# Kernel optimization log

Measured on AMD Instinct MI355X. Metric: run time of the kernel, lower is better.

The kernel has to match this reference:

```python
import jax, jax.numpy as jnp
import numpy as np

T, B, IN_DIM = 512, 256, 256
H1, H = 512, 256          # fc hidden, GRU hidden
OUT_DIM = 18


def setup_inputs() -> dict:
    key = jax.random.key(0)
    ks = jax.random.split(key, 14)
    s = 0.05
    return {
        "x":      jax.random.normal(ks[0], (T, B, IN_DIM), dtype=jnp.float32),
        # fc1: Linear(IN_DIM,H1)+ReLU, Linear(H1,H)+ReLU
        "W_fc1a": jax.random.normal(ks[1], (H1, IN_DIM), dtype=jnp.float32) * s,
        "b_fc1a": jax.random.normal(ks[2], (H1,), dtype=jnp.float32) * s,
        "W_fc1b": jax.random.normal(ks[3], (H, H1), dtype=jnp.float32) * s,
        "b_fc1b": jax.random.normal(ks[4], (H,), dtype=jnp.float32) * s,
        # GRUCell(H, H): weights ordered [r, z, n] like torch
        "W_ih":   jax.random.normal(ks[5], (3 * H, H), dtype=jnp.float32) * s,
        "b_ih":   jax.random.normal(ks[6], (3 * H,), dtype=jnp.float32) * s,
        "W_hh":   jax.random.normal(ks[7], (3 * H, H), dtype=jnp.float32) * s,
        "b_hh":   jax.random.normal(ks[8], (3 * H,), dtype=jnp.float32) * s,
        # fc2: Linear(H,H1)+ReLU, Linear(H1,OUT_DIM)
        "W_fc2a": jax.random.normal(ks[9], (H1, H), dtype=jnp.float32) * s,
        "b_fc2a": jax.random.normal(ks[10], (H1,), dtype=jnp.float32) * s,
        "W_fc2b": jax.random.normal(ks[11], (OUT_DIM, H1), dtype=jnp.float32) * s,
        "b_fc2b": jax.random.normal(ks[12], (OUT_DIM,), dtype=jnp.float32) * s,
    }


def reference(x, W_fc1a, b_fc1a, W_fc1b, b_fc1b,
              W_ih, b_ih, W_hh, b_hh,
              W_fc2a, b_fc2a, W_fc2b, b_fc2b):
    batch = x.shape[1]
    h0 = jnp.zeros((batch, W_hh.shape[1]), dtype=x.dtype)

    def step(h, xt):
        # fc1 MLP
        a = jax.nn.relu(xt @ W_fc1a.T + b_fc1a)
        a = jax.nn.relu(a @ W_fc1b.T + b_fc1b)
        # GRUCell (torch gate order r, z, n)
        gi = a @ W_ih.T + b_ih            # [B, 3H]
        gh = h @ W_hh.T + b_hh            # [B, 3H]
        i_r, i_z, i_n = jnp.split(gi, 3, axis=-1)
        h_r, h_z, h_n = jnp.split(gh, 3, axis=-1)
        r = jax.nn.sigmoid(i_r + h_r)
        z = jax.nn.sigmoid(i_z + h_z)
        n = jnp.tanh(i_n + r * h_n)
        h_new = (1.0 - z) * n + z * h
        # fc2 head
        q = jax.nn.relu(h_new @ W_fc2a.T + b_fc2a) @ W_fc2b.T + b_fc2b
        return h_new, q

    _, qs = jax.lax.scan(step, h0, x)     # qs: [T, B, OUT_DIM]
    return qs
```

## Files before the change

### kernel.cpp

```cpp
#include <hip/hip_runtime.h>
#include <hip/hip_fp16.h>
#include <cstdio>

typedef unsigned short u16;
typedef __attribute__((ext_vector_type(8))) _Float16 f16x8;
typedef __attribute__((ext_vector_type(4))) float fv4;

#define TT 512
#define BB 256

__device__ __forceinline__ float us2f(u16 u) {
    union { u16 u; _Float16 h; } c; c.u = u; return (float)c.h;
}
__device__ __forceinline__ u16 f2us(float f) {
    union { u16 u; _Float16 h; } c; c.h = (_Float16)f; return c.u;
}

__device__ __forceinline__ void gl_lds16(const u16* g, u16* l) {
    __builtin_amdgcn_global_load_lds(
        (const __attribute__((address_space(1))) void*)g,
        (__attribute__((address_space(3))) void*)l, 16, 0, 0);
}

__global__ void cvt_f32_f16(const float* __restrict__ s, u16* __restrict__ d, int n) {
    long stride = (long)gridDim.x * blockDim.x * 8;
    for (long i = ((long)blockIdx.x * blockDim.x + threadIdx.x) * 8; i < n; i += stride) {
        f16x8 o;
#pragma unroll
        for (int j = 0; j < 8; ++j) o[j] = (_Float16)s[i + j];
        *(f16x8*)(d + i) = o;
    }
}

__global__ void bias_fold(const float* __restrict__ bih, const float* __restrict__ bhh,
                          float* __restrict__ bsum) {
    int i = blockIdx.x * blockDim.x + threadIdx.x;
    if (i < 768) bsum[i] = bih[i] + (i < 512 ? bhh[i] : 0.f);
}

__global__ void pack_whh(const float* __restrict__ W, u16* __restrict__ Wp) {
    int t = blockIdx.x * blockDim.x + threadIdx.x;
    int l = t & 63;
    int kt = (t >> 6) & 7;
    int jt = t >> 9;
    int j = jt * 16 + (l & 15);
    int k = kt * 32 + (l >> 4) * 8;
    f16x8 o;
#pragma unroll
    for (int i = 0; i < 8; ++i) o[i] = (_Float16)W[j * 256 + k + i];
    *(f16x8*)(Wp + (size_t)t * 8) = o;
}

__global__ void pack_w2b(const float* __restrict__ W, u16* __restrict__ Wp) {
    int t = blockIdx.x * blockDim.x + threadIdx.x;
    int l = t & 63;
    int kt = (t >> 6) & 15;
    int nt = t >> 10;
    int n = nt * 16 + (l & 15);
    int k = kt * 32 + (l >> 4) * 8;
    f16x8 o;
#pragma unroll
    for (int i = 0; i < 8; ++i)
        o[i] = (n < 18) ? (_Float16)W[n * 512 + k + i] : (_Float16)0.f;
    *(f16x8*)(Wp + (size_t)t * 8) = o;
}

__global__ __launch_bounds__(256) void gemm_bt(
    const u16* __restrict__ A, const u16* __restrict__ B,
    const float* __restrict__ bias, u16* __restrict__ C,
    int N, int K, int act)
{
    __shared__ u16 Ash[4096] __attribute__((aligned(16)));
    __shared__ u16 Bsh[4096] __attribute__((aligned(16)));
    const int tid = threadIdx.x;
    const int l = tid & 63, w = tid >> 6;
    const long m0 = (long)blockIdx.y * 128;
    const int n0 = blockIdx.x * 128;
    const int r = tid >> 2, c8 = (tid & 3) * 8;
    const u16* gA0 = A + (m0 + r) * K + c8;
    const u16* gA1 = A + (m0 + 64 + r) * K + c8;
    const u16* gB0 = B + (long)(n0 + r) * K + c8;
    const u16* gB1 = B + (long)(n0 + 64 + r) * K + c8;
    const int mb = (w >> 1) * 64, nb = (w & 1) * 64;
    const int mrow = l & 15, colq = (l >> 4) * 8;
    fv4 acc[4][4] = {};
    for (int k0 = 0; k0 < K; k0 += 32) {
        gl_lds16(gA0 + k0, &Ash[tid * 8]);
        gl_lds16(gA1 + k0, &Ash[2048 + tid * 8]);
        gl_lds16(gB0 + k0, &Bsh[tid * 8]);
        gl_lds16(gB1 + k0, &Bsh[2048 + tid * 8]);
        __syncthreads();
        f16x8 af[4], bf[4];
#pragma unroll
        for (int i = 0; i < 4; ++i)
            af[i] = *(const f16x8*)&Ash[(mb + i * 16 + mrow) * 32 + colq];
#pragma unroll
        for (int i = 0; i < 4; ++i)
            bf[i] = *(const f16x8*)&Bsh[(nb + i * 16 + mrow) * 32 + colq];
#pragma unroll
        for (int mt = 0; mt < 4; ++mt)
#pragma unroll
            for (int nt = 0; nt < 4; ++nt)
                acc[mt][nt] = __builtin_amdgcn_mfma_f32_16x16x32_f16(
                    af[mt], bf[nt], acc[mt][nt], 0, 0, 0);
        __syncthreads();
    }
    float bv[4];
#pragma unroll
    for (int nt = 0; nt < 4; ++nt) bv[nt] = bias[n0 + nb + nt * 16 + mrow];
    const int rq = (l >> 4) * 4;
#pragma unroll
    for (int mt = 0; mt < 4; ++mt)
#pragma unroll
        for (int nt = 0; nt < 4; ++nt)
#pragma unroll
            for (int i = 0; i < 4; ++i) {
                float v = acc[mt][nt][i] + bv[nt];
                if (act) v = fmaxf(v, 0.f);
                C[(m0 + mb + mt * 16 + rq + i) * (long)N + (n0 + nb + nt * 16 + mrow)] = f2us(v);
            }
}

__global__ __launch_bounds__(256) void gemm_gi(
    const u16* __restrict__ A, const u16* __restrict__ B,
    const float* __restrict__ bias, u16* __restrict__ GIp)
{
    __shared__ u16 Ash[4096] __attribute__((aligned(16)));
    __shared__ u16 Bsh[4096] __attribute__((aligned(16)));
    const int tid = threadIdx.x;
    const int l = tid & 63, w = tid >> 6;
    const long m0 = (long)blockIdx.y * 128;
    const int n0 = blockIdx.x * 128;
    const int r = tid >> 2, c8 = (tid & 3) * 8;
    const u16* gA0 = A + (m0 + r) * 256 + c8;
    const u16* gA1 = A + (m0 + 64 + r) * 256 + c8;
    const u16* gB0 = B + (long)(n0 + r) * 256 + c8;
    const u16* gB1 = B + (long)(n0 + 64 + r) * 256 + c8;
    const int mb = (w >> 1) * 64, nb = (w & 1) * 64;
    const int mrow = l & 15, colq = (l >> 4) * 8;
    fv4 acc[4][4] = {};
    for (int k0 = 0; k0 < 256; k0 += 32) {
        gl_lds16(gA0 + k0, &Ash[tid * 8]);
        gl_lds16(gA1 + k0, &Ash[2048 + tid * 8]);
        gl_lds16(gB0 + k0, &Bsh[tid * 8]);
        gl_lds16(gB1 + k0, &Bsh[2048 + tid * 8]);
        __syncthreads();
        f16x8 af[4], bf[4];
#pragma unroll
        for (int i = 0; i < 4; ++i)
            af[i] = *(const f16x8*)&Ash[(mb + i * 16 + mrow) * 32 + colq];
#pragma unroll
        for (int i = 0; i < 4; ++i)
            bf[i] = *(const f16x8*)&Bsh[(nb + i * 16 + mrow) * 32 + colq];
#pragma unroll
        for (int mt = 0; mt < 4; ++mt)
#pragma unroll
            for (int nt = 0; nt < 4; ++nt)
                acc[mt][nt] = __builtin_amdgcn_mfma_f32_16x16x32_f16(
                    af[mt], bf[nt], acc[mt][nt], 0, 0, 0);
        __syncthreads();
    }
    float bv[4];
#pragma unroll
    for (int nt = 0; nt < 4; ++nt) bv[nt] = bias[n0 + nb + nt * 16 + mrow];
    const int rq = (l >> 4) * 4;
#pragma unroll
    for (int mt = 0; mt < 4; ++mt)
#pragma unroll
        for (int nt = 0; nt < 4; ++nt)
#pragma unroll
            for (int i = 0; i < 4; ++i) {
                float v = acc[mt][nt][i] + bv[nt];
                int m = (int)(m0 + mb + mt * 16 + rq + i);
                int n = n0 + nb + nt * 16 + mrow;
                int t  = m >> 8, b = m & 255;
                int blk = b >> 4, rb = b & 15, q = rb >> 2, i2 = rb & 3;
                int g = n >> 8, c = n & 255, w2 = c >> 5, s = (c >> 4) & 1, cl = c & 15;
                size_t idx = ((((size_t)t * 16 + blk) * 8 + w2) * 64 + (q * 16 + cl)) * 24
                             + (g * 2 + s) * 4 + i2;
                GIp[idx] = f2us(v);
            }
}

__global__ __launch_bounds__(512, 2) void gru_seq5(
    const u16* __restrict__ Wp, const u16* __restrict__ GIp,
    const float* __restrict__ bhh, u16* __restrict__ Hp)
{
    __shared__ u16 h_sh[2][4096] __attribute__((aligned(16)));
    __shared__ u16 Wl[49152] __attribute__((aligned(16)));
    const int tid = threadIdx.x;
    const int l = tid & 63, w = tid >> 6;
    const int blk = blockIdx.x;
    const int col = l & 15, quad = l >> 4;

    for (int i = tid; i < 4096; i += 512) h_sh[0][i] = 0;
    for (int idx = tid; idx < 6144; idx += 512) {
        int kt6 = idx / 3072, rem = idx % 3072;
        *(f16x8*)&Wl[(size_t)idx * 8] =
            *(const f16x8*)&Wp[(((size_t)(rem >> 6) * 8 + 6 + kt6) * 64 + (rem & 63)) * 8];
    }

    int jts[6];
#pragma unroll
    for (int g = 0; g < 3; ++g)
#pragma unroll
        for (int s = 0; s < 2; ++s) jts[g * 2 + s] = g * 16 + 2 * w + s;

    f16x8 wf[6][6];
#pragma unroll
    for (int u = 0; u < 6; ++u)
#pragma unroll
        for (int kt = 0; kt < 6; ++kt)
            wf[u][kt] = *(const f16x8*)&Wp[(((size_t)jts[u] * 8 + kt) * 64 + l) * 8];
#pragma unroll
    for (int u = 0; u < 6; ++u)
#pragma unroll
        for (int kt = 0; kt < 6; ++kt)
            asm volatile("" : "+v"(wf[u][kt]));

    float hbn[2] = { bhh[512 + 32 * w + col], bhh[512 + 32 * w + 16 + col] };

    const u16* gbase = GIp + ((size_t)(blk * 8 + w) * 64 + l) * 24;
    f16x8 gcur[3], gnxt[3];
#pragma unroll
    for (int j = 0; j < 3; ++j) gcur[j] = *(const f16x8*)(gbase + j * 8);

    float hold[2][4] = {};
    u16* hp_base = Hp + (size_t)blk * 4096 + tid * 8;
    __syncthreads();

    for (int t = 0; t < TT; ++t) {
        const int rd = t & 1, wr = (t + 1) & 1;
        if (t) {
            f16x8 hv = *(const f16x8*)&h_sh[rd][tid * 8];
            *(f16x8*)(hp_base + (size_t)(t - 1) * 65536) = hv;
        }
        const u16* gn = gbase + (size_t)(t < TT - 1 ? t + 1 : t) * 196608;
#pragma unroll
        for (int j = 0; j < 3; ++j) gnxt[j] = *(const f16x8*)(gn + j * 8);

        fv4 acc[6] = {};
#pragma unroll
        for (int kt = 0; kt < 6; ++kt) {
            f16x8 a = *(const f16x8*)&h_sh[rd][(kt * 64 + l) * 8];
#pragma unroll
            for (int u = 0; u < 6; ++u)
                acc[u] = __builtin_amdgcn_mfma_f32_16x16x32_f16(a, wf[u][kt], acc[u], 0, 0, 0);
        }
#pragma unroll
        for (int kt6 = 0; kt6 < 2; ++kt6) {
            f16x8 a = *(const f16x8*)&h_sh[rd][((6 + kt6) * 64 + l) * 8];
#pragma unroll
            for (int u = 0; u < 6; ++u) {
                f16x8 bw = *(const f16x8*)&Wl[((size_t)(kt6 * 48 + jts[u]) * 64 + l) * 8];
                acc[u] = __builtin_amdgcn_mfma_f32_16x16x32_f16(a, bw, acc[u], 0, 0, 0);
            }
        }
#pragma unroll
        for (int s = 0; s < 2; ++s) {
            const int q2 = s * 2 + (col >> 3);
#pragma unroll
            for (int i = 0; i < 4; ++i) {
                float pr  = (float)gcur[0][s * 4 + i] + acc[0 + s][i];
                float pz  = (float)gcur[1][s * 4 + i] + acc[2 + s][i];
                float h_n = acc[4 + s][i] + hbn[s];
                float rg = __builtin_amdgcn_rcpf(1.f + __expf(-pr));
                float zg = __builtin_amdgcn_rcpf(1.f + __expf(-pz));
                float pre = (float)gcur[2][s * 4 + i] + rg * h_n;
                float ea = __expf(-2.f * fabsf(pre));
                float th = (1.f - ea) * __builtin_amdgcn_rcpf(1.f + ea);
                float ng = (pre >= 0.f) ? th : -th;
                float hn = (1.f - zg) * ng + zg * hold[s][i];
                hold[s][i] = hn;
                h_sh[wr][(w * 64 + q2 * 16 + quad * 4 + i) * 8 + (col & 7)] = f2us(hn);
            }
        }
#pragma unroll
        for (int j = 0; j < 3; ++j) gcur[j] = gnxt[j];
        __syncthreads();
    }
    {
        f16x8 hv = *(const f16x8*)&h_sh[0][tid * 8];
        *(f16x8*)(hp_base + (size_t)511 * 65536) = hv;
    }
}

__global__ __launch_bounds__(256) void gemm_hp(
    const u16* __restrict__ Hp, const u16* __restrict__ B,
    const float* __restrict__ bias, u16* __restrict__ C)
{
    __shared__ u16 Bsh[4096] __attribute__((aligned(16)));
    const int tid = threadIdx.x;
    const int l = tid & 63, w = tid >> 6;
    const long m0 = (long)blockIdx.y * 128;
    const int n0 = blockIdx.x * 128;
    const int r = tid >> 2, c8 = (tid & 3) * 8;
    const u16* gB0 = B + (long)(n0 + r) * 256 + c8;
    const u16* gB1 = B + (long)(n0 + 64 + r) * 256 + c8;
    const int mb = (w >> 1) * 64, nb = (w & 1) * 64;
    const int mrow = l & 15, colq = (l >> 4) * 8;
    const int t = (int)(m0 >> 8), half = ((int)m0 >> 7) & 1;
    const u16* aBase = Hp + ((size_t)t * 16 + half * 8 + (mb >> 4)) * 4096 + (size_t)l * 8;
    fv4 acc[4][4] = {};
    for (int k0 = 0; k0 < 256; k0 += 32) {
        gl_lds16(gB0 + k0, &Bsh[tid * 8]);
        gl_lds16(gB1 + k0, &Bsh[2048 + tid * 8]);
        const int kt = k0 >> 5;
        f16x8 af[4];
#pragma unroll
        for (int i = 0; i < 4; ++i)
            af[i] = *(const f16x8*)(aBase + (size_t)i * 4096 + kt * 512);
        __syncthreads();
        f16x8 bf[4];
#pragma unroll
        for (int i = 0; i < 4; ++i)
            bf[i] = *(const f16x8*)&Bsh[(nb + i * 16 + mrow) * 32 + colq];
#pragma unroll
        for (int mt = 0; mt < 4; ++mt)
#pragma unroll
            for (int nt = 0; nt < 4; ++nt)
                acc[mt][nt] = __builtin_amdgcn_mfma_f32_16x16x32_f16(
                    af[mt], bf[nt], acc[mt][nt], 0, 0, 0);
        __syncthreads();
    }
    float bv[4];
#pragma unroll
    for (int nt = 0; nt < 4; ++nt) bv[nt] = bias[n0 + nb + nt * 16 + mrow];
    const int rq = (l >> 4) * 4;
#pragma unroll
    for (int mt = 0; mt < 4; ++mt)
#pragma unroll
        for (int nt = 0; nt < 4; ++nt)
#pragma unroll
            for (int i = 0; i < 4; ++i) {
                float v = fmaxf(acc[mt][nt][i] + bv[nt], 0.f);
                C[(m0 + mb + mt * 16 + rq + i) * 512L + (n0 + nb + nt * 16 + mrow)] = f2us(v);
            }
}

__global__ __launch_bounds__(256) void head_gemm(
    const u16* __restrict__ Q1, const u16* __restrict__ W2p,
    const float* __restrict__ b2, float* __restrict__ out)
{
    __shared__ u16 Ash[4096] __attribute__((aligned(16)));
    __shared__ u16 Bsh[16384] __attribute__((aligned(16)));
    const int tid = threadIdx.x;
    const int l = tid & 63, w = tid >> 6;
    const long m0 = (long)blockIdx.x * 128;
    const int col = l & 15, quad = l >> 4, colq = quad * 8;
    for (int i = tid * 8; i < 16384; i += 2048)
        *(f16x8*)&Bsh[i] = *(const f16x8*)&W2p[i];
    const int r = tid >> 2, c8 = (tid & 3) * 8;
    const u16* gA0 = Q1 + (m0 + r) * 512 + c8;
    const u16* gA1 = Q1 + (m0 + 64 + r) * 512 + c8;
    fv4 acc[2][2] = {};
    for (int k0 = 0; k0 < 512; k0 += 32) {
        gl_lds16(gA0 + k0, &Ash[tid * 8]);
        gl_lds16(gA1 + k0, &Ash[2048 + tid * 8]);
        __syncthreads();
        const int kt = k0 >> 5;
        f16x8 af[2], bf[2];
#pragma unroll
        for (int mt = 0; mt < 2; ++mt)
            af[mt] = *(const f16x8*)&Ash[(w * 32 + mt * 16 + col) * 32 + colq];
#pragma unroll
        for (int nt = 0; nt < 2; ++nt)
            bf[nt] = *(const f16x8*)&Bsh[((nt * 16 + kt) * 64 + l) * 8];
#pragma unroll
        for (int mt = 0; mt < 2; ++mt)
#pragma unroll
            for (int nt = 0; nt < 2; ++nt)
                acc[mt][nt] = __builtin_amdgcn_mfma_f32_16x16x32_f16(
                    af[mt], bf[nt], acc[mt][nt], 0, 0, 0);
        __syncthreads();
    }
    const int rq = quad * 4;
#pragma unroll
    for (int nt = 0; nt < 2; ++nt) {
        int c = nt * 16 + col;
        if (c < 18) {
            float bias = b2[c];
#pragma unroll
            for (int mt = 0; mt < 2; ++mt)
#pragma unroll
                for (int i = 0; i < 4; ++i)
                    out[(m0 + w * 32 + mt * 16 + rq + i) * 18 + c] = acc[mt][nt][i] + bias;
        }
    }
}

extern "C" void kernel_launch(void* const* d_in, const int* in_sizes, int n_in,
                              void* d_out, int out_size, void* d_ws, size_t ws_size,
                              hipStream_t stream) {
    const float* x   = (const float*)d_in[0];
    const float* W1a = (const float*)d_in[1];
    const float* b1a = (const float*)d_in[2];
    const float* W1b = (const float*)d_in[3];
    const float* b1b = (const float*)d_in[4];
    const float* Wih = (const float*)d_in[5];
    const float* bih = (const float*)d_in[6];
    const float* Whh = (const float*)d_in[7];
    const float* bhh = (const float*)d_in[8];
    const float* W2a = (const float*)d_in[9];
    const float* b2a = (const float*)d_in[10];
    const float* W2b = (const float*)d_in[11];
    const float* b2b = (const float*)d_in[12];

    char* ws = (char*)d_ws;
    u16* R    = (u16*)ws;
    u16* A2b  = (u16*)(ws + 201326592);
    u16* XH   = (u16*)(ws + 268435456);
    float* bsum = (float*)(ws + 268435456 + 67108864 - 4096);
    u16* W1ah = (u16*)(ws + 335544320);
    u16* W1bh = (u16*)(ws + 335806464);
    u16* Wihh = (u16*)(ws + 336068608);
    u16* W2ah = (u16*)(ws + 336461824);
    u16* Wpk  = (u16*)(ws + 336723968);
    u16* W2p  = (u16*)(ws + 337117184);
    if (ws_size < 337149952) {
        fprintf(stderr, "kernel_launch: ws too small (%zu < 337149952)\n", ws_size);
    }

    cvt_f32_f16<<<dim3(2048), dim3(256), 0, stream>>>(x, XH, 33554432);
    cvt_f32_f16<<<dim3(64), dim3(256), 0, stream>>>(W1a, W1ah, 131072);
    cvt_f32_f16<<<dim3(64), dim3(256), 0, stream>>>(W1b, W1bh, 131072);
    cvt_f32_f16<<<dim3(96), dim3(256), 0, stream>>>(Wih, Wihh, 196608);
    cvt_f32_f16<<<dim3(64), dim3(256), 0, stream>>>(W2a, W2ah, 131072);
    pack_whh<<<dim3(96), dim3(256), 0, stream>>>(Whh, Wpk);
    pack_w2b<<<dim3(8), dim3(256), 0, stream>>>(W2b, W2p);

    gemm_bt<<<dim3(4, 1024), dim3(256), 0, stream>>>(XH, W1ah, b1a, R,   512, 256, 1);
    bias_fold<<<dim3(3), dim3(256), 0, stream>>>(bih, bhh, bsum);
    gemm_bt<<<dim3(2, 1024), dim3(256), 0, stream>>>(R,  W1bh, b1b, A2b, 256, 512, 1);
    gemm_gi<<<dim3(6, 1024), dim3(256), 0, stream>>>(A2b, Wihh, bsum, R);
    gru_seq5<<<dim3(16), dim3(512), 0, stream>>>(Wpk, R, bhh, XH);
    gemm_hp<<<dim3(4, 1024), dim3(256), 0, stream>>>(XH, W2ah, b2a, R);
    head_gemm<<<dim3(1024), dim3(256), 0, stream>>>(R, W2p, b2b, (float*)d_out);
}
```

Before: 1.569 ms.

## Split GRU recurrent step across 16 waves per block instead of 8

The sequential GRU kernel now launches 1024 threads per block, so each wave owns one 16-column tile per gate instead of two. Per-wave register weights halve, MFMA chains per step shrink from 48 to 24, and the gate loads narrow to 4-wide halves. The tanh is also rewritten in a cheaper exp/rcp form and the state update becomes a single fma-style blend. This shortens the per-timestep critical path of the latency-bound recurrence, at the cost of a barrier over twice as many waves each step.

```diff
diff --git a/kernel.cpp b/kernel.cpp
--- a/kernel.cpp
+++ b/kernel.cpp
@@ -4,6 +4,7 @@
 
 typedef unsigned short u16;
 typedef __attribute__((ext_vector_type(8))) _Float16 f16x8;
+typedef __attribute__((ext_vector_type(4))) _Float16 f16x4;
 typedef __attribute__((ext_vector_type(4))) float fv4;
 
 #define TT 512
@@ -182,7 +183,7 @@
             }
 }
 
-__global__ __launch_bounds__(512, 2) void gru_seq5(
+__global__ __launch_bounds__(1024) void gru_seq7(
     const u16* __restrict__ Wp, const u16* __restrict__ GIp,
     const float* __restrict__ bhh, u16* __restrict__ Hp)
 {
@@ -193,93 +194,85 @@
     const int blk = blockIdx.x;
     const int col = l & 15, quad = l >> 4;
 
-    for (int i = tid; i < 4096; i += 512) h_sh[0][i] = 0;
-    for (int idx = tid; idx < 6144; idx += 512) {
+    for (int i = tid; i < 4096; i += 1024) h_sh[0][i] = 0;
+    for (int idx = tid; idx < 6144; idx += 1024) {
         int kt6 = idx / 3072, rem = idx % 3072;
         *(f16x8*)&Wl[(size_t)idx * 8] =
             *(const f16x8*)&Wp[(((size_t)(rem >> 6) * 8 + 6 + kt6) * 64 + (rem & 63)) * 8];
     }
 
-    int jts[6];
-#pragma unroll
-    for (int g = 0; g < 3; ++g)
-#pragma unroll
-        for (int s = 0; s < 2; ++s) jts[g * 2 + s] = g * 16 + 2 * w + s;
-
-    f16x8 wf[6][6];
-#pragma unroll
-    for (int u = 0; u < 6; ++u)
-#pragma unroll
-        for (int kt = 0; kt < 6; ++kt)
-            wf[u][kt] = *(const f16x8*)&Wp[(((size_t)jts[u] * 8 + kt) * 64 + l) * 8];
-#pragma unroll
-    for (int u = 0; u < 6; ++u)
-#pragma unroll
-        for (int kt = 0; kt < 6; ++kt)
-            asm volatile("" : "+v"(wf[u][kt]));
-
-    float hbn[2] = { bhh[512 + 32 * w + col], bhh[512 + 32 * w + 16 + col] };
-
-    const u16* gbase = GIp + ((size_t)(blk * 8 + w) * 64 + l) * 24;
-    f16x8 gcur[3], gnxt[3];
-#pragma unroll
-    for (int j = 0; j < 3; ++j) gcur[j] = *(const f16x8*)(gbase + j * 8);
-
-    float hold[2][4] = {};
+    const int jt0 = w, jt1 = 16 + w, jt2 = 32 + w;
+
+    f16x8 wf[3][6];
+    {
+        const int jts[3] = { jt0, jt1, jt2 };
+#pragma unroll
+        for (int g = 0; g < 3; ++g)
+#pragma unroll
+            for (int kt = 0; kt < 6; ++kt)
+                wf[g][kt] = *(const f16x8*)&Wp[(((size_t)jts[g] * 8 + kt) * 64 + l) * 8];
+    }
+
+    const int c = 16 * w + col;
+    const float hbn = bhh[512 + c];
+
+    const u16* gbase = GIp + ((size_t)(blk * 8 + (w >> 1)) * 64 + l) * 24 + (w & 1) * 4;
+    f16x4 gcur[3], gnxt[3];
+#pragma unroll
+    for (int g = 0; g < 3; ++g) gcur[g] = *(const f16x4*)(gbase + g * 8);
+
+    float hold[4] = {};
     u16* hp_base = Hp + (size_t)blk * 4096 + tid * 8;
+    const int wbase = ((w >> 1) * 64 + ((2 * w + (col >> 3)) & 3) * 16 + quad * 4) * 8 + (col & 7);
     __syncthreads();
 
     for (int t = 0; t < TT; ++t) {
         const int rd = t & 1, wr = (t + 1) & 1;
-        if (t) {
+        if (t && tid < 512) {
             f16x8 hv = *(const f16x8*)&h_sh[rd][tid * 8];
             *(f16x8*)(hp_base + (size_t)(t - 1) * 65536) = hv;
         }
         const u16* gn = gbase + (size_t)(t < TT - 1 ? t + 1 : t) * 196608;
 #pragma unroll
-        for (int j = 0; j < 3; ++j) gnxt[j] = *(const f16x8*)(gn + j * 8);
-
-        fv4 acc[6] = {};
+        for (int g = 0; g < 3; ++g) gnxt[g] = *(const f16x4*)(gn + g * 8);
+
+        fv4 acc[3] = {};
 #pragma unroll
         for (int kt = 0; kt < 6; ++kt) {
             f16x8 a = *(const f16x8*)&h_sh[rd][(kt * 64 + l) * 8];
-#pragma unroll
-            for (int u = 0; u < 6; ++u)
-                acc[u] = __builtin_amdgcn_mfma_f32_16x16x32_f16(a, wf[u][kt], acc[u], 0, 0, 0);
+            acc[0] = __builtin_amdgcn_mfma_f32_16x16x32_f16(a, wf[0][kt], acc[0], 0, 0, 0);
+            acc[1] = __builtin_amdgcn_mfma_f32_16x16x32_f16(a, wf[1][kt], acc[1], 0, 0, 0);
+            acc[2] = __builtin_amdgcn_mfma_f32_16x16x32_f16(a, wf[2][kt], acc[2], 0, 0, 0);
         }
 #pragma unroll
         for (int kt6 = 0; kt6 < 2; ++kt6) {
             f16x8 a = *(const f16x8*)&h_sh[rd][((6 + kt6) * 64 + l) * 8];
-#pragma unroll
-            for (int u = 0; u < 6; ++u) {
-                f16x8 bw = *(const f16x8*)&Wl[((size_t)(kt6 * 48 + jts[u]) * 64 + l) * 8];
-                acc[u] = __builtin_amdgcn_mfma_f32_16x16x32_f16(a, bw, acc[u], 0, 0, 0);
-            }
+            f16x8 b0 = *(const f16x8*)&Wl[((size_t)(kt6 * 48 + jt0) * 64 + l) * 8];
+            f16x8 b1 = *(const f16x8*)&Wl[((size_t)(kt6 * 48 + jt1) * 64 + l) * 8];
+            f16x8 b2 = *(const f16x8*)&Wl[((size_t)(kt6 * 48 + jt2) * 64 + l) * 8];
+            acc[0] = __builtin_amdgcn_mfma_f32_16x16x32_f16(a, b0, acc[0], 0, 0, 0);
+            acc[1] = __builtin_amdgcn_mfma_f32_16x16x32_f16(a, b1, acc[1], 0, 0, 0);
+            acc[2] = __builtin_amdgcn_mfma_f32_16x16x32_f16(a, b2, acc[2], 0, 0, 0);
         }
 #pragma unroll
-        for (int s = 0; s < 2; ++s) {
-            const int q2 = s * 2 + (col >> 3);
-#pragma unroll
-            for (int i = 0; i < 4; ++i) {
-                float pr  = (float)gcur[0][s * 4 + i] + acc[0 + s][i];
-                float pz  = (float)gcur[1][s * 4 + i] + acc[2 + s][i];
-                float h_n = acc[4 + s][i] + hbn[s];
-                float rg = __builtin_amdgcn_rcpf(1.f + __expf(-pr));
-                float zg = __builtin_amdgcn_rcpf(1.f + __expf(-pz));
-                float pre = (float)gcur[2][s * 4 + i] + rg * h_n;
-                float ea = __expf(-2.f * fabsf(pre));
-                float th = (1.f - ea) * __builtin_amdgcn_rcpf(1.f + ea);
-                float ng = (pre >= 0.f) ? th : -th;
-                float hn = (1.f - zg) * ng + zg * hold[s][i];
-                hold[s][i] = hn;
-                h_sh[wr][(w * 64 + q2 * 16 + quad * 4 + i) * 8 + (col & 7)] = f2us(hn);
-            }
+        for (int i = 0; i < 4; ++i) {
+            float pr  = (float)gcur[0][i] + acc[0][i];
+            float pz  = (float)gcur[1][i] + acc[1][i];
+            float hnp = acc[2][i] + hbn;
+            float rg = __builtin_amdgcn_rcpf(1.f + __expf(-pr));
+            float zg = __builtin_amdgcn_rcpf(1.f + __expf(-pz));
+            float pre = (float)gcur[2][i] + rg * hnp;
+            float e2 = __expf(2.f * pre);
+            float ng = 1.f - 2.f * __builtin_amdgcn_rcpf(e2 + 1.f);
+            float hn = ng + zg * (hold[i] - ng);
+            hold[i] = hn;
+            h_sh[wr][wbase + i * 8] = f2us(hn);
         }
 #pragma unroll
-        for (int j = 0; j < 3; ++j) gcur[j] = gnxt[j];
-        __syncthreads();
-    }
-    {
+        for (int g = 0; g < 3; ++g) gcur[g] = gnxt[g];
+        __syncthreads();
+    }
+    if (tid < 512) {
         f16x8 hv = *(const f16x8*)&h_sh[0][tid * 8];
         *(f16x8*)(hp_base + (size_t)511 * 65536) = hv;
     }
@@ -433,7 +426,7 @@
     bias_fold<<<dim3(3), dim3(256), 0, stream>>>(bih, bhh, bsum);
     gemm_bt<<<dim3(2, 1024), dim3(256), 0, stream>>>(R,  W1bh, b1b, A2b, 256, 512, 1);
     gemm_gi<<<dim3(6, 1024), dim3(256), 0, stream>>>(A2b, Wihh, bsum, R);
-    gru_seq5<<<dim3(16), dim3(512), 0, stream>>>(Wpk, R, bhh, XH);
+    gru_seq7<<<dim3(16), dim3(1024), 0, stream>>>(Wpk, R, bhh, XH);
     gemm_hp<<<dim3(4, 1024), dim3(256), 0, stream>>>(XH, W2ah, b2a, R);
     head_gemm<<<dim3(1024), dim3(256), 0, stream>>>(R, W2p, b2b, (float*)d_out);
 }
```

After: 1.392 ms. 11.3% less time.
